# Kernel optimization log

Hardware: AMD Instinct MI355X
Metric: run time of the kernel (lower is better)

The kernel has to match this reference:

```python
import jax, jax.numpy as jnp
import numpy as np

N_HEADS = 16


def setup_inputs() -> dict:
    key = jax.random.key(0)
    ks = jax.random.split(key, 9)
    B, S, D = 4, 2048, 1024
    query = jax.random.normal(ks[0], (B, S, D), dtype=jnp.float32)
    key_t = jax.random.normal(ks[1], (B, S, D), dtype=jnp.float32)
    value = jax.random.normal(ks[2], (B, S, D), dtype=jnp.float32)
    mask = jax.random.randint(ks[3], (B, 1, S, S), 0, 10) > 0
    scale_w = 0.02  # keep exp(attention) in a safe range
    Wq = jax.random.normal(ks[4], (D, D), dtype=jnp.float32) * scale_w
    Wk = jax.random.normal(ks[5], (D, D), dtype=jnp.float32) * scale_w
    Wv = jax.random.normal(ks[6], (D, D), dtype=jnp.float32) * scale_w
    fc_w = jax.random.normal(ks[7], (D, D), dtype=jnp.float32) * scale_w
    fc_b = jnp.zeros((D,), dtype=jnp.float32)
    return {"query": query, "key": key_t, "value": value, "mask": mask,
            "Wq": Wq, "Wk": Wk, "Wv": Wv, "fc_w": fc_w, "fc_b": fc_b}


def reference(query, key, value, mask, Wq, Wk, Wv, fc_w, fc_b):
    B, S, D = query.shape
    H = N_HEADS
    Dh = D // H
    scale = jnp.sqrt(jnp.asarray(D / H, dtype=query.dtype))
    # Faithful to original: direct reshape [B,S,D] -> [B,H,S,Dh] (no transpose)
    Q = (query @ Wq.T).reshape(B, H, S, Dh)
    K = (key @ Wk.T).reshape(B, H, S, Dh)
    V = (value @ Wv.T).reshape(B, H, S, Dh)
    attn = jnp.einsum('bhqd,bhkd->bhqk', Q, K) / scale  # [B,H,S,S]
    # Hand-rolled masked softmax: exp, masked_fill(False->0), normalize, nan->0
    temp = jnp.where(mask, jnp.exp(attn), 0.0)
    attn = temp / jnp.sum(temp, axis=-1, keepdims=True)
    attn = jnp.where(jnp.isnan(attn), 0.0, attn)
    res = jnp.einsum('bhqk,bhkd->bhqd', attn, V)  # [B,H,S,Dh]
    outs = res.transpose(0, 2, 1, 3).reshape(B, S, D)
    outs = outs @ fc_w.T + fc_b
    return outs, res.transpose(1, 0, 2, 3)
```

## Files before the change

### kernel.cpp

```cpp
#include <hip/hip_runtime.h>


typedef __attribute__((ext_vector_type(8))) short bf16x8;
typedef __attribute__((ext_vector_type(4))) short bf16x4;
typedef __attribute__((ext_vector_type(4))) float f32x4;

#define MFMA32(a, b, c) __builtin_amdgcn_mfma_f32_16x16x32_bf16(a, b, c, 0, 0, 0)

static __device__ __forceinline__ float fast_exp2(float x) {
#if __has_builtin(__builtin_amdgcn_exp2f)
  return __builtin_amdgcn_exp2f(x);
#else
  return __expf(x * 0.69314718056f);
#endif
}

__device__ __forceinline__ unsigned short fbf(float f) {
  union { float f; unsigned u; } x; x.f = f;
  unsigned r = x.u + 0x7fffu + ((x.u >> 16) & 1u);
  return (unsigned short)(r >> 16);
}

static __device__ __forceinline__ bf16x4 pack2(unsigned lo, unsigned hi) {
  union { unsigned u[2]; bf16x4 v; } x; x.u[0] = lo; x.u[1] = hi; return x.v;
}

static __device__ __forceinline__ bf16x8 cat2(bf16x4 lo, bf16x4 hi) {
  union { bf16x4 h[2]; bf16x8 v; } x; x.h[0] = lo; x.h[1] = hi; return x.v;
}

static __device__ __forceinline__ bf16x4 epp(f32x4 s, unsigned pre, int sh) {
  union { float f; unsigned u; } e0, e1, e2, e3;
  e0.f = fast_exp2(s[0]); e1.f = fast_exp2(s[1]);
  e2.f = fast_exp2(s[2]); e3.f = fast_exp2(s[3]);
  unsigned p01 = __builtin_amdgcn_perm(e1.u + 0x8000u, e0.u + 0x8000u, 0x07060302u);
  unsigned p23 = __builtin_amdgcn_perm(e3.u + 0x8000u, e2.u + 0x8000u, 0x07060302u);
  int m0 = __builtin_amdgcn_sbfe(pre, sh + 0, 1), m1 = __builtin_amdgcn_sbfe(pre, sh + 1, 1);
  int m2 = __builtin_amdgcn_sbfe(pre, sh + 2, 1), m3 = __builtin_amdgcn_sbfe(pre, sh + 3, 1);
  unsigned k01 = __builtin_amdgcn_perm((unsigned)m1, (unsigned)m0, 0x07060100u);
  unsigned k23 = __builtin_amdgcn_perm((unsigned)m3, (unsigned)m2, 0x07060100u);
  return pack2(p01 & k01, p23 & k23);
}

__global__ __launch_bounds__(256) void f2b3_kernel(const float* __restrict__ s0,
                                                   const float* __restrict__ s1,
                                                   const float* __restrict__ s2,
                                                   unsigned short* __restrict__ d0,
                                                   unsigned short* __restrict__ d1,
                                                   unsigned short* __restrict__ d2) {
  int z = blockIdx.y;
  const float* s = (z == 0) ? s0 : (z == 1) ? s1 : s2;
  unsigned short* d = (z == 0) ? d0 : (z == 1) ? d1 : d2;
  int i = blockIdx.x * 256 + threadIdx.x;
  float4 v = ((const float4*)s)[i];
  ushort4 o;
  o.x = fbf(v.x); o.y = fbf(v.y); o.z = fbf(v.z); o.w = fbf(v.w);
  ((ushort4*)d)[i] = o;
}

__global__ __launch_bounds__(256) void f2b4_kernel(const float* __restrict__ s0,
                                                   const float* __restrict__ s1,
                                                   const float* __restrict__ s2,
                                                   const float* __restrict__ s3,
                                                   unsigned short* __restrict__ d0,
                                                   unsigned short* __restrict__ d1,
                                                   unsigned short* __restrict__ d2,
                                                   unsigned short* __restrict__ d3) {
  int z = blockIdx.y;
  const float* s = (z == 0) ? s0 : (z == 1) ? s1 : (z == 2) ? s2 : s3;
  unsigned short* d = (z == 0) ? d0 : (z == 1) ? d1 : (z == 2) ? d2 : d3;
  int i = blockIdx.x * 256 + threadIdx.x;
  float4 v = ((const float4*)s)[i];
  ushort4 o;
  o.x = fbf(v.x); o.y = fbf(v.y); o.z = fbf(v.z); o.w = fbf(v.w);
  ((ushort4*)d)[i] = o;
}

__global__ __launch_bounds__(256) void pack_mask_kernel(const int* __restrict__ m,
                                                        unsigned long long* __restrict__ o) {
  int i = blockIdx.x * 256 + threadIdx.x;
  unsigned long long b = __ballot(m[i] != 0);
  if ((threadIdx.x & 63) == 0) {
    int row = i >> 11;
    int kt = (i >> 7) & 15;
    int h = (i >> 6) & 1;
    o[(kt * 8192 + row) * 2 + h] = b;
  }
}

__global__ __launch_bounds__(256) void proj_kernel(const unsigned short* __restrict__ A0,
                                                   const unsigned short* __restrict__ A1,
                                                   const unsigned short* __restrict__ A2,
                                                   const unsigned short* __restrict__ W0,
                                                   const unsigned short* __restrict__ W1,
                                                   const unsigned short* __restrict__ W2,
                                                   unsigned short* __restrict__ C0,
                                                   unsigned short* __restrict__ C1,
                                                   unsigned short* __restrict__ C2) {
  __shared__ unsigned short Alds[128 * 32];
  __shared__ unsigned short Blds[128 * 32];
  const int z = blockIdx.z;
  const unsigned short* A = (z == 0) ? A0 : (z == 1) ? A1 : A2;
  const unsigned short* B = (z == 0) ? W0 : (z == 1) ? W1 : W2;
  const int tid = threadIdx.x;
  const int w = tid >> 6, l = tid & 63, q4 = l >> 4, c16 = l & 15;
  const int wm = w & 1, wn = w >> 1;
  const int mBase = blockIdx.y * 128, nBase = blockIdx.x * 128;

  f32x4 acc[4][4];
#pragma unroll
  for (int a0 = 0; a0 < 4; ++a0)
#pragma unroll
    for (int a1 = 0; a1 < 4; ++a1) acc[a0][a1] = (f32x4){0.f, 0.f, 0.f, 0.f};

  const int r0 = tid >> 2, cc0 = tid & 3;

  for (int kt = 0; kt < 32; ++kt) {
    __syncthreads();
    const unsigned short* ga0 = A + (mBase + r0) * 1024 + kt * 32 + cc0 * 8;
    const unsigned short* ga1 = A + (mBase + 64 + r0) * 1024 + kt * 32 + cc0 * 8;
    const unsigned short* gb0 = B + (nBase + r0) * 1024 + kt * 32 + cc0 * 8;
    const unsigned short* gb1 = B + (nBase + 64 + r0) * 1024 + kt * 32 + cc0 * 8;
    __builtin_amdgcn_global_load_lds((const __attribute__((address_space(1))) void*)ga0,
                                     (__attribute__((address_space(3))) void*)(&Alds[tid * 8]),
                                     16, 0, 0);
    __builtin_amdgcn_global_load_lds((const __attribute__((address_space(1))) void*)ga1,
                                     (__attribute__((address_space(3))) void*)(&Alds[(tid + 256) * 8]),
                                     16, 0, 0);
    __builtin_amdgcn_global_load_lds((const __attribute__((address_space(1))) void*)gb0,
                                     (__attribute__((address_space(3))) void*)(&Blds[tid * 8]),
                                     16, 0, 0);
    __builtin_amdgcn_global_load_lds((const __attribute__((address_space(1))) void*)gb1,
                                     (__attribute__((address_space(3))) void*)(&Blds[(tid + 256) * 8]),
                                     16, 0, 0);
    __syncthreads();

    bf16x8 af[4], bfr[4];
#pragma unroll
    for (int mi = 0; mi < 4; ++mi)
      af[mi] = *(const bf16x8*)&Alds[(wm * 64 + mi * 16 + c16) * 32 + q4 * 8];
#pragma unroll
    for (int ni = 0; ni < 4; ++ni)
      bfr[ni] = *(const bf16x8*)&Blds[(wn * 64 + ni * 16 + c16) * 32 + q4 * 8];
#pragma unroll
    for (int mi = 0; mi < 4; ++mi)
#pragma unroll
      for (int ni = 0; ni < 4; ++ni) acc[mi][ni] = MFMA32(af[mi], bfr[ni], acc[mi][ni]);
  }

  const float scale = (z == 0) ? 0.18033688f : 1.0f;
#pragma unroll
  for (int mi = 0; mi < 4; ++mi) {
#pragma unroll
    for (int ni = 0; ni < 4; ++ni) {
#pragma unroll
      for (int rg = 0; rg < 4; ++rg) {
        int row = mBase + wm * 64 + mi * 16 + q4 * 4 + rg;
        int col = nBase + wn * 64 + ni * 16 + c16;
        float v = acc[mi][ni][rg];
        if (z < 2) {
          unsigned short* C = (z == 0) ? C0 : C1;
          C[row * 1024 + col] = fbf(v * scale);
        } else {
          int bb = row >> 11, rr = row & 2047;
          int hh = rr >> 7;
          int ss = ((rr & 127) << 4) | (col >> 6);
          int dh = col & 63;
          C2[((bb * 16 + hh) * 64 + dh) * 2048 + ss] = fbf(v);
        }
      }
    }
  }
}

__global__ __launch_bounds__(256) void gemm_out(const unsigned short* __restrict__ A,
                                                const unsigned short* __restrict__ B,
                                                float* __restrict__ C,
                                                const float* __restrict__ bias) {
  __shared__ unsigned short Alds[128 * 32];
  __shared__ unsigned short Blds[128 * 32];
  const int tid = threadIdx.x;
  const int w = tid >> 6, l = tid & 63, q4 = l >> 4, c16 = l & 15;
  const int wm = w & 1, wn = w >> 1;
  const int mBase = blockIdx.y * 128, nBase = blockIdx.x * 128;

  f32x4 acc[4][4];
#pragma unroll
  for (int a0 = 0; a0 < 4; ++a0)
#pragma unroll
    for (int a1 = 0; a1 < 4; ++a1) acc[a0][a1] = (f32x4){0.f, 0.f, 0.f, 0.f};

  const int r0 = tid >> 2, cc0 = tid & 3;

  for (int kt = 0; kt < 32; ++kt) {
    __syncthreads();
    const unsigned short* ga0 = A + (mBase + r0) * 1024 + kt * 32 + cc0 * 8;
    const unsigned short* ga1 = A + (mBase + 64 + r0) * 1024 + kt * 32 + cc0 * 8;
    const unsigned short* gb0 = B + (nBase + r0) * 1024 + kt * 32 + cc0 * 8;
    const unsigned short* gb1 = B + (nBase + 64 + r0) * 1024 + kt * 32 + cc0 * 8;
    __builtin_amdgcn_global_load_lds((const __attribute__((address_space(1))) void*)ga0,
                                     (__attribute__((address_space(3))) void*)(&Alds[tid * 8]),
                                     16, 0, 0);
    __builtin_amdgcn_global_load_lds((const __attribute__((address_space(1))) void*)ga1,
                                     (__attribute__((address_space(3))) void*)(&Alds[(tid + 256) * 8]),
                                     16, 0, 0);
    __builtin_amdgcn_global_load_lds((const __attribute__((address_space(1))) void*)gb0,
                                     (__attribute__((address_space(3))) void*)(&Blds[tid * 8]),
                                     16, 0, 0);
    __builtin_amdgcn_global_load_lds((const __attribute__((address_space(1))) void*)gb1,
                                     (__attribute__((address_space(3))) void*)(&Blds[(tid + 256) * 8]),
                                     16, 0, 0);
    __syncthreads();

    bf16x8 af[4], bfr[4];
#pragma unroll
    for (int mi = 0; mi < 4; ++mi)
      af[mi] = *(const bf16x8*)&Alds[(wm * 64 + mi * 16 + c16) * 32 + q4 * 8];
#pragma unroll
    for (int ni = 0; ni < 4; ++ni)
      bfr[ni] = *(const bf16x8*)&Blds[(wn * 64 + ni * 16 + c16) * 32 + q4 * 8];
#pragma unroll
    for (int mi = 0; mi < 4; ++mi)
#pragma unroll
      for (int ni = 0; ni < 4; ++ni) acc[mi][ni] = MFMA32(af[mi], bfr[ni], acc[mi][ni]);
  }

#pragma unroll
  for (int mi = 0; mi < 4; ++mi) {
#pragma unroll
    for (int ni = 0; ni < 4; ++ni) {
#pragma unroll
      for (int rg = 0; rg < 4; ++rg) {
        int row = mBase + wm * 64 + mi * 16 + q4 * 4 + rg;
        int col = nBase + wn * 64 + ni * 16 + c16;
        C[row * 1024 + col] = acc[mi][ni][rg] + bias[col];
      }
    }
  }
}

__global__ __launch_bounds__(256, 4) void flash_kernel(const unsigned short* __restrict__ Q,
                                                       const unsigned short* __restrict__ K,
                                                       const unsigned short* __restrict__ Vt,
                                                       const uint4* __restrict__ mb,
                                                       unsigned short* __restrict__ Cws,
                                                       float* __restrict__ res2) {
  __shared__ unsigned short Klds[128 * 64];
  __shared__ unsigned short Vtlds[64 * 128];
  const int tid = threadIdx.x;
  const int w = tid >> 6, l = tid & 63, q4 = l >> 4, c16 = l & 15;
  const int q44 = q4 * 4;
  const int qt = blockIdx.x, h = blockIdx.y, b = blockIdx.z;
  const unsigned short* Qh = Q + (b * 2048 + h * 128) * 1024;
  const unsigned short* Kh = K + (b * 2048 + h * 128) * 1024;
  const unsigned short* Vth = Vt + (b * 16 + h) * 64 * 2048;

  bf16x8 qf[2][2];
#pragma unroll
  for (int i = 0; i < 2; ++i)
#pragma unroll
    for (int kc = 0; kc < 2; ++kc)
      qf[i][kc] = *(const bf16x8*)(Qh + (qt * 128 + w * 32 + i * 16 + c16) * 64 + kc * 32 + q4 * 8);

  const int rowi = b * 2048 + qt * 128 + w * 32 + c16;

  const int kOff = (tid >> 3) * 64 + (((tid & 7) ^ ((tid >> 3) & 7)) * 8);
  const int vOff = (tid >> 4) * 2048 + (((tid & 15) ^ (tid >> 4)) * 8);

  const int kb0 = c16 * 64 + ((q4 ^ (c16 & 7)) * 8);
  const int kb1 = kb0 ^ 32;
  const int vb = c16 * 128 + (q4 & 1) * 4;
  const int q41 = q4 >> 1;

  const bf16x8 ones8 = {(short)0x3F80, (short)0x3F80, (short)0x3F80, (short)0x3F80,
                        (short)0x3F80, (short)0x3F80, (short)0x3F80, (short)0x3F80};

  f32x4 oacc[2][4], soacc[2];
#pragma unroll
  for (int i = 0; i < 2; ++i) {
    soacc[i] = (f32x4){0.f, 0.f, 0.f, 0.f};
#pragma unroll
    for (int t = 0; t < 4; ++t) oacc[i][t] = (f32x4){0.f, 0.f, 0.f, 0.f};
  }

  for (int kt = 0; kt < 16; ++kt) {
    const unsigned short* gk = Kh + kt * 8192 + kOff;
    const unsigned short* gv = Vth + kt * 128 + vOff;
#pragma unroll
    for (int j = 0; j < 4; ++j) {
      __builtin_amdgcn_global_load_lds((const __attribute__((address_space(1))) void*)(gk + j * 2048),
                                       (__attribute__((address_space(3))) void*)(&Klds[(j * 256 + tid) * 8]),
                                       16, 0, 0);
      __builtin_amdgcn_global_load_lds((const __attribute__((address_space(1))) void*)(gv + j * 32768),
                                       (__attribute__((address_space(3))) void*)(&Vtlds[(j * 256 + tid) * 8]),
                                       16, 0, 0);
    }
    uint4 m0 = mb[kt * 8192 + rowi];
    uint4 m1 = mb[kt * 8192 + rowi + 16];
    unsigned pre0[4] = {m0.x >> q44, m0.y >> q44, m0.z >> q44, m0.w >> q44};
    unsigned pre1[4] = {m1.x >> q44, m1.y >> q44, m1.z >> q44, m1.w >> q44};
    __syncthreads();

#pragma unroll
    for (int m = 0; m < 4; ++m) {
      bf16x8 kfE0 = *(const bf16x8*)(Klds + kb0 + (2 * m) * 1024);
      bf16x8 kfE1 = *(const bf16x8*)(Klds + kb1 + (2 * m) * 1024);
      bf16x8 kfO0 = *(const bf16x8*)(Klds + kb0 + (2 * m + 1) * 1024);
      bf16x8 kfO1 = *(const bf16x8*)(Klds + kb1 + (2 * m + 1) * 1024);
      f32x4 sE0 = {0.f, 0.f, 0.f, 0.f}, sE1 = {0.f, 0.f, 0.f, 0.f};
      f32x4 sO0 = {0.f, 0.f, 0.f, 0.f}, sO1 = {0.f, 0.f, 0.f, 0.f};
      sE0 = MFMA32(kfE0, qf[0][0], sE0); sE0 = MFMA32(kfE1, qf[0][1], sE0);
      sE1 = MFMA32(kfE0, qf[1][0], sE1); sE1 = MFMA32(kfE1, qf[1][1], sE1);
      sO0 = MFMA32(kfO0, qf[0][0], sO0); sO0 = MFMA32(kfO1, qf[0][1], sO0);
      sO1 = MFMA32(kfO0, qf[1][0], sO1); sO1 = MFMA32(kfO1, qf[1][1], sO1);

      int shE = 0, shO = 16;
      bf16x8 pf0 = cat2(epp(sE0, pre0[m], shE), epp(sO0, pre0[m], shO));
      bf16x8 pf1 = cat2(epp(sE1, pre1[m], shE), epp(sO1, pre1[m], shO));

      int pLo = (4 * m + q41) ^ c16;
      int aLo = vb + pLo * 8;
#pragma unroll
      for (int t = 0; t < 4; ++t) {
        bf16x4 vlo = *(const bf16x4*)(Vtlds + aLo + t * 2048);
        bf16x4 vhi = *(const bf16x4*)(Vtlds + (aLo ^ 16) + t * 2048);
        bf16x8 vf8 = cat2(vlo, vhi);
        oacc[0][t] = MFMA32(vf8, pf0, oacc[0][t]);
        oacc[1][t] = MFMA32(vf8, pf1, oacc[1][t]);
      }
      soacc[0] = MFMA32(ones8, pf0, soacc[0]);
      soacc[1] = MFMA32(ones8, pf1, soacc[1]);
    }
    __syncthreads();
  }

#pragma unroll
  for (int i = 0; i < 2; ++i) {
    float sum = soacc[i][0];
    float rcp = (sum > 0.f) ? (1.0f / sum) : 0.f;
    int q = qt * 128 + w * 32 + i * 16 + c16;
    float* rp = res2 + (((h * 4 + b) * 2048 + q) * 64 + q44);
    unsigned short* cp = Cws + ((b * 2048 + q) * 1024 + h * 64 + q44);
#pragma unroll
    for (int t = 0; t < 4; ++t) {
      float o0 = oacc[i][t][0] * rcp, o1 = oacc[i][t][1] * rcp;
      float o2 = oacc[i][t][2] * rcp, o3 = oacc[i][t][3] * rcp;
      float4 fo = {o0, o1, o2, o3};
      *(float4*)(rp + t * 16) = fo;
      ushort4 cv = {fbf(o0), fbf(o1), fbf(o2), fbf(o3)};
      *(ushort4*)(cp + t * 16) = cv;
    }
  }
}

extern "C" void kernel_launch(void* const* d_in, const int* in_sizes, int n_in,
                              void* d_out, int out_size, void* d_ws, size_t ws_size,
                              hipStream_t stream) {
  const float* query = (const float*)d_in[0];
  const float* key_t = (const float*)d_in[1];
  const float* value = (const float*)d_in[2];
  const int* mask = (const int*)d_in[3];
  const float* Wq = (const float*)d_in[4];
  const float* Wk = (const float*)d_in[5];
  const float* Wv = (const float*)d_in[6];
  const float* fcw = (const float*)d_in[7];
  const float* fcb = (const float*)d_in[8];
  float* out = (float*)d_out;

  char* ws = (char*)d_ws;
  unsigned short* qbf = (unsigned short*)(ws);
  unsigned short* kbf = (unsigned short*)(ws + (16u << 20));
  unsigned short* vbf = (unsigned short*)(ws + (32u << 20));
  unsigned short* wqb = (unsigned short*)(ws + (48u << 20));
  unsigned short* wkb = (unsigned short*)(ws + (50u << 20));
  unsigned short* wvb = (unsigned short*)(ws + (52u << 20));
  unsigned short* fwb = (unsigned short*)(ws + (54u << 20));
  unsigned short* Qf = (unsigned short*)(ws + (56u << 20));
  unsigned short* Kf = (unsigned short*)(ws + (72u << 20));
  unsigned short* Vt = (unsigned short*)(ws + (88u << 20));
  unsigned short* Cws = qbf;
  unsigned long long* mbits = (unsigned long long*)kbf;

  f2b3_kernel<<<dim3(8192, 3), 256, 0, stream>>>(query, key_t, value, qbf, kbf, vbf);
  f2b4_kernel<<<dim3(1024, 4), 256, 0, stream>>>(Wq, Wk, Wv, fcw, wqb, wkb, wvb, fwb);

  proj_kernel<<<dim3(8, 64, 3), 256, 0, stream>>>(qbf, kbf, vbf, wqb, wkb, wvb, Qf, Kf, Vt);

  pack_mask_kernel<<<65536, 256, 0, stream>>>(mask, mbits);

  flash_kernel<<<dim3(16, 16, 4), 256, 0, stream>>>(Qf, Kf, Vt, (const uint4*)mbits, Cws,
                                                    out + 8388608);

  gemm_out<<<dim3(8, 64), 256, 0, stream>>>(Cws, fwb, out, fcb);
}
```

Measured before the change: 465.7 us.

## Split V transpose into separate kernel and remap block order for XCD locality

```diff
diff --git a/kernel.cpp b/kernel.cpp
--- a/kernel.cpp
+++ b/kernel.cpp
@@ -88,6 +88,32 @@
   }
 }
 
+__global__ __launch_bounds__(256) void vtrans_kernel(const unsigned short* __restrict__ Vf,
+                                                     unsigned short* __restrict__ Vt) {
+  __shared__ unsigned short T[64][72];
+  const int bh = blockIdx.y;
+  const int s0 = blockIdx.x * 64;
+  const int tid = threadIdx.x;
+  {
+    int r = tid >> 2, c = (tid & 3) * 16;
+    const unsigned short* src = Vf + bh * 131072 + (s0 + r) * 64 + c;
+    uint4 v0 = *(const uint4*)(src);
+    uint4 v1 = *(const uint4*)(src + 8);
+    *(uint4*)&T[r][c] = v0;
+    *(uint4*)&T[r][c + 8] = v1;
+  }
+  __syncthreads();
+  {
+    int dh = tid & 63, rb = (tid >> 6) * 16;
+    unsigned short o[16];
+#pragma unroll
+    for (int j = 0; j < 16; ++j) o[j] = T[rb + j][dh];
+    unsigned short* dst = Vt + bh * 131072 + dh * 2048 + s0 + rb;
+    *(uint4*)dst = *(const uint4*)&o[0];
+    *(uint4*)(dst + 8) = *(const uint4*)&o[8];
+  }
+}
+
 __global__ __launch_bounds__(256) void proj_kernel(const unsigned short* __restrict__ A0,
                                                    const unsigned short* __restrict__ A1,
                                                    const unsigned short* __restrict__ A2,
@@ -99,13 +125,17 @@
                                                    unsigned short* __restrict__ C2) {
   __shared__ unsigned short Alds[128 * 32];
   __shared__ unsigned short Blds[128 * 32];
-  const int z = blockIdx.z;
+  const int flat = (blockIdx.z * 64 + blockIdx.y) * 8 + blockIdx.x;
+  const int wid = (flat & 7) * 192 + (flat >> 3);
+  const int z = wid >> 9;
+  const int by = (wid >> 3) & 63;
+  const int bx = wid & 7;
   const unsigned short* A = (z == 0) ? A0 : (z == 1) ? A1 : A2;
   const unsigned short* B = (z == 0) ? W0 : (z == 1) ? W1 : W2;
   const int tid = threadIdx.x;
   const int w = tid >> 6, l = tid & 63, q4 = l >> 4, c16 = l & 15;
   const int wm = w & 1, wn = w >> 1;
-  const int mBase = blockIdx.y * 128, nBase = blockIdx.x * 128;
+  const int mBase = by * 128, nBase = bx * 128;
 
   f32x4 acc[4][4];
 #pragma unroll
@@ -148,6 +178,7 @@
       for (int ni = 0; ni < 4; ++ni) acc[mi][ni] = MFMA32(af[mi], bfr[ni], acc[mi][ni]);
   }
 
+  unsigned short* C = (z == 0) ? C0 : (z == 1) ? C1 : C2;
   const float scale = (z == 0) ? 0.18033688f : 1.0f;
 #pragma unroll
   for (int mi = 0; mi < 4; ++mi) {
@@ -157,17 +188,7 @@
       for (int rg = 0; rg < 4; ++rg) {
         int row = mBase + wm * 64 + mi * 16 + q4 * 4 + rg;
         int col = nBase + wn * 64 + ni * 16 + c16;
-        float v = acc[mi][ni][rg];
-        if (z < 2) {
-          unsigned short* C = (z == 0) ? C0 : C1;
-          C[row * 1024 + col] = fbf(v * scale);
-        } else {
-          int bb = row >> 11, rr = row & 2047;
-          int hh = rr >> 7;
-          int ss = ((rr & 127) << 4) | (col >> 6);
-          int dh = col & 63;
-          C2[((bb * 16 + hh) * 64 + dh) * 2048 + ss] = fbf(v);
-        }
+        C[row * 1024 + col] = fbf(acc[mi][ni][rg] * scale);
       }
     }
   }
@@ -179,10 +200,13 @@
                                                 const float* __restrict__ bias) {
   __shared__ unsigned short Alds[128 * 32];
   __shared__ unsigned short Blds[128 * 32];
+  const int flat = blockIdx.y * 8 + blockIdx.x;
+  const int wid = (flat & 7) * 64 + (flat >> 3);
+  const int by = wid >> 3, bx = wid & 7;
   const int tid = threadIdx.x;
   const int w = tid >> 6, l = tid & 63, q4 = l >> 4, c16 = l & 15;
   const int wm = w & 1, wn = w >> 1;
-  const int mBase = blockIdx.y * 128, nBase = blockIdx.x * 128;
+  const int mBase = by * 128, nBase = bx * 128;
 
   f32x4 acc[4][4];
 #pragma unroll
@@ -250,7 +274,9 @@
   const int tid = threadIdx.x;
   const int w = tid >> 6, l = tid & 63, q4 = l >> 4, c16 = l & 15;
   const int q44 = q4 * 4;
-  const int qt = blockIdx.x, h = blockIdx.y, b = blockIdx.z;
+  const int flat = (blockIdx.z * 16 + blockIdx.y) * 16 + blockIdx.x;
+  const int wid = (flat & 7) * 128 + (flat >> 3);
+  const int qt = wid & 15, h = (wid >> 4) & 15, b = wid >> 8;
   const unsigned short* Qh = Q + (b * 2048 + h * 128) * 1024;
   const unsigned short* Kh = K + (b * 2048 + h * 128) * 1024;
   const unsigned short* Vth = Vt + (b * 16 + h) * 64 * 2048;
@@ -377,14 +403,17 @@
   unsigned short* fwb = (unsigned short*)(ws + (54u << 20));
   unsigned short* Qf = (unsigned short*)(ws + (56u << 20));
   unsigned short* Kf = (unsigned short*)(ws + (72u << 20));
-  unsigned short* Vt = (unsigned short*)(ws + (88u << 20));
+  unsigned short* Vnat = (unsigned short*)(ws + (88u << 20));
   unsigned short* Cws = qbf;
   unsigned long long* mbits = (unsigned long long*)kbf;
+  unsigned short* Vt = vbf;
 
   f2b3_kernel<<<dim3(8192, 3), 256, 0, stream>>>(query, key_t, value, qbf, kbf, vbf);
   f2b4_kernel<<<dim3(1024, 4), 256, 0, stream>>>(Wq, Wk, Wv, fcw, wqb, wkb, wvb, fwb);
 
-  proj_kernel<<<dim3(8, 64, 3), 256, 0, stream>>>(qbf, kbf, vbf, wqb, wkb, wvb, Qf, Kf, Vt);
+  proj_kernel<<<dim3(8, 64, 3), 256, 0, stream>>>(qbf, kbf, vbf, wqb, wkb, wvb, Qf, Kf, Vnat);
+
+  vtrans_kernel<<<dim3(32, 64), 256, 0, stream>>>(Vnat, Vt);
 
   pack_mask_kernel<<<65536, 256, 0, stream>>>(mask, mbits);
 
```

Result: faster. 408.6 us (-12.3%).
